# Performance work log

Measured on AMD Instinct MI355X. Metric: run time of the kernel, lower is better.

## Reference

```python
import jax, jax.numpy as jnp
import numpy as np
from jax import lax

W = 50      # window size
EPS = 1e-5  # BatchNorm eps (torch default)


def setup_inputs() -> dict:
    key = jax.random.key(0)
    ks = jax.random.split(key, 40)
    def n(i, shape, s=0.1):
        return (jax.random.normal(ks[i], shape, dtype=jnp.float32) * s).astype(jnp.float32)
    inp = {}
    inp['x'] = jax.random.normal(ks[0], (16, 1, 2048), dtype=jnp.float32)
    # conv stack (eval-mode BatchNorm: running mean/var are params)
    inp['conv1_w'] = n(1, (64, 1, 9));  inp['conv1_b'] = n(2, (64,))
    inp['bn1_g'] = 1.0 + n(3, (64,));   inp['bn1_b'] = n(4, (64,))
    inp['bn1_m'] = n(5, (64,));         inp['bn1_v'] = 0.5 + jax.random.uniform(ks[6], (64,), dtype=jnp.float32)
    inp['conv2_w'] = n(7, (32, 64, 7)); inp['conv2_b'] = n(8, (32,))
    inp['bn2_g'] = 1.0 + n(9, (32,));   inp['bn2_b'] = n(10, (32,))
    inp['bn2_m'] = n(11, (32,));        inp['bn2_v'] = 0.5 + jax.random.uniform(ks[12], (32,), dtype=jnp.float32)
    inp['conv3_w'] = n(13, (16, 32, 5)); inp['conv3_b'] = n(14, (16,))
    inp['bn3_g'] = 1.0 + n(15, (16,));   inp['bn3_b'] = n(16, (16,))
    inp['bn3_m'] = n(17, (16,));         inp['bn3_v'] = 0.5 + jax.random.uniform(ks[18], (16,), dtype=jnp.float32)
    # 2-layer LSTM, hidden 64, input 16 (torch gate order i,f,g,o)
    H = 64
    inp['wih0'] = n(19, (4 * H, 16)); inp['whh0'] = n(20, (4 * H, H))
    inp['bih0'] = n(21, (4 * H,));    inp['bhh0'] = n(22, (4 * H,))
    inp['wih1'] = n(23, (4 * H, H));  inp['whh1'] = n(24, (4 * H, H))
    inp['bih1'] = n(25, (4 * H,));    inp['bhh1'] = n(26, (4 * H,))
    # classifier 64 -> 32 -> 2
    inp['fc1_w'] = n(27, (32, H)); inp['fc1_b'] = n(28, (32,))
    inp['fc2_w'] = n(29, (2, 32)); inp['fc2_b'] = n(30, (2,))
    return inp


def _conv1d(x, w, b, pad):
    # x: [N, Cin, L], w: [Cout, Cin, K]
    y = lax.conv_general_dilated(x, w, (1,), [(pad, pad)],
                                 dimension_numbers=('NCH', 'OIH', 'NCH'))
    return y + b[:, None]


def _bn(x, g, b, m, v):
    # eval-mode BatchNorm1d over channel dim of [N, C, L]
    return (x - m[:, None]) * (g / jnp.sqrt(v + EPS))[:, None] + b[:, None]


def _lstm_layer(x, wih, whh, bih, bhh):
    # x: [B, T, D] -> [B, T, H]; torch gate order (i, f, g, o)
    B, T, D = x.shape
    H = whh.shape[1]
    xs = jnp.transpose(x, (1, 0, 2))                     # [T, B, D]
    pre = xs @ wih.T + (bih + bhh)                       # [T, B, 4H] input projection, hoisted
    def step(carry, p):
        h, c = carry
        g = p + h @ whh.T
        i, f, gg, o = jnp.split(g, 4, axis=-1)
        c = jax.nn.sigmoid(f) * c + jax.nn.sigmoid(i) * jnp.tanh(gg)
        h = jax.nn.sigmoid(o) * jnp.tanh(c)
        return (h, c), h
    h0 = jnp.zeros((B, H), x.dtype)
    _, hs = lax.scan(step, (h0, h0), pre)
    return jnp.transpose(hs, (1, 0, 2))


def reference(x, conv1_w, conv1_b, bn1_g, bn1_b, bn1_m, bn1_v,
              conv2_w, conv2_b, bn2_g, bn2_b, bn2_m, bn2_v,
              conv3_w, conv3_b, bn3_g, bn3_b, bn3_m, bn3_v,
              wih0, whh0, bih0, bhh0, wih1, whh1, bih1, bhh1,
              fc1_w, fc1_b, fc2_w, fc2_b):
    B, C, T = x.shape
    # sliding windows with left zero-pad of W-1 -> [B, T, C, W]
    xp = jnp.pad(x, ((0, 0), (0, 0), (W - 1, 0)))
    idx = jnp.arange(T)[:, None] + jnp.arange(W)[None, :]  # [T, W]
    win = xp[:, :, idx]                                    # [B, C, T, W]
    win = jnp.transpose(win, (0, 2, 1, 3)).reshape(B * T, C, W)
    # conv -> BN(eval) -> ReLU stack (dropout is identity in eval)
    h = jax.nn.relu(_bn(_conv1d(win, conv1_w, conv1_b, 4), bn1_g, bn1_b, bn1_m, bn1_v))
    h = jax.nn.relu(_bn(_conv1d(h, conv2_w, conv2_b, 3), bn2_g, bn2_b, bn2_m, bn2_v))
    h = jax.nn.relu(_bn(_conv1d(h, conv3_w, conv3_b, 2), bn3_g, bn3_b, bn3_m, bn3_v))
    feats = h.mean(axis=-1).reshape(B, T, -1)              # AdaptiveAvgPool1d(1) -> [B, T, 16]
    # 2-layer LSTM
    h1 = _lstm_layer(feats, wih0, whh0, bih0, bhh0)
    h2 = _lstm_layer(h1, wih1, whh1, bih1, bhh1)           # [B, T, 64]
    # classifier
    z = jax.nn.relu(h2 @ fc1_w.T + fc1_b)
    logits = z @ fc2_w.T + fc2_b                           # [B, T, 2]
    return logits
```

## Files before the change

### kernel.cpp

```cpp
#include <hip/hip_runtime.h>

#define EPSV 1e-5f
#define SCOPE_AGENT __HIP_MEMORY_SCOPE_AGENT

__device__ __forceinline__ float fast_rcp(float x) { return __builtin_amdgcn_rcpf(x); }
__device__ __forceinline__ float tanhfast(float x) {
    float e = __expf(2.0f * x);
    return 1.0f - 2.0f * fast_rcp(e + 1.0f);
}
__device__ __forceinline__ float dot4(const float4 w, const float4 v, float a) {
    a = fmaf(w.x, v.x, a);
    a = fmaf(w.y, v.y, a);
    a = fmaf(w.z, v.z, a);
    a = fmaf(w.w, v.w, a);
    return a;
}
#define DPPF(v, ctrl) __int_as_float(__builtin_amdgcn_mov_dpp(__float_as_int(v), (ctrl), 0xF, 0xF, false))

typedef unsigned long long ull;

struct Rec2S {
    float hbuf0[2][80];
    float hbuf1[2][80];
    float xst[16][80];
};
struct EdgeS {
    float A1[64 * 36];
    float A2[32 * 36];
    float xl[16], xr[16];
    float s1[64], t1[64], s2[32], t2[32], s3[16], t3[16];
    float psumE[288];
    float pi[512];
};

__global__ void pack_kernel(const float* __restrict__ w2, const float* __restrict__ w3,
                            float* __restrict__ w2t2, float4* __restrict__ w3p4,
                            float* __restrict__ w3p1, int* __restrict__ sync_ints) {
    int j = blockIdx.x * 256 + threadIdx.x;
    if (j < 16384) {
        int i = j >> 8;
        int o = (j >> 3) & 31;
        int k = j & 7;
        w2t2[j] = (k < 7) ? w2[o * 448 + i * 7 + k] : 0.0f;
    } else if (j < 16896) {
        int e = j - 16384;
        int i = e >> 4, o = e & 15;
        int base = o * 160 + i * 5;
        w3p4[e] = make_float4(w3[base], w3[base + 1], w3[base + 2], w3[base + 3]);
        w3p1[e] = w3[base + 4];
    } else if (j < 16896 + 4096) {
        sync_ints[j - 16896] = 0;
    }
}

__global__ __launch_bounds__(256) void conv1f_kernel(
    const float* __restrict__ x, const float* __restrict__ w1,
    const float* __restrict__ b1, const float* __restrict__ g1,
    const float* __restrict__ be1, const float* __restrict__ m1,
    const float* __restrict__ vv1, float* __restrict__ a1f)
{
    __shared__ float xs[72];
    const int tid = threadIdx.x;
    const int T = blockIdx.x * 64;
    const int b = blockIdx.y;
    if (tid < 72) {
        int gi = T - 49 + tid;
        xs[tid] = (gi >= 0 && gi < 2048) ? x[b * 2048 + gi] : 0.0f;
    }
    const int i = tid & 63, q = tid >> 6;
    float wv[9];
    #pragma unroll
    for (int k = 0; k < 9; ++k) wv[k] = w1[i * 9 + k];
    float sc = g1[i] * rsqrtf(vv1[i] + EPSV);
    float tc = (b1[i] - m1[i]) * sc + be1[i];
// ... 98 lines not shown
        float av[12] = {R0.x, R0.y, R0.z, R0.w, R1.x, R1.y, R1.z, R1.w,
                        R2.x, R2.y, R2.z, R2.w};
        float4 wa = w3p4[i * 16 + o];
        float w4 = w3p1[i * 16 + o];
        #pragma unroll
        for (int q = 0; q < 8; ++q) {
            acc[q] = fmaf(wa.x, av[q], acc[q]);
            acc[q] = fmaf(wa.y, av[q + 1], acc[q]);
            acc[q] = fmaf(wa.z, av[q + 2], acc[q]);
            acc[q] = fmaf(wa.w, av[q + 3], acc[q]);
            acc[q] = fmaf(w4,   av[q + 4], acc[q]);
        }
    }
    #pragma unroll
    for (int q = 0; q < 8; ++q) {
        int v3 = T + pg * 8 + q;
        if (v3 < 2079)
            a3f[((long)b * 2080 + v3) * 16 + o] = fmaxf(acc[q] * sc + tc, 0.0f);
        else if (v3 < 2080)
            a3f[((long)b * 2080 + v3) * 16 + o] = 0.0f;
    }
}

__device__ void rec_merged(char* smemraw, int b,
    const float* __restrict__ feats,
    const float* __restrict__ wih0, const float* __restrict__ whh0,
    const float* __restrict__ bih0, const float* __restrict__ bhh0,
    const float* __restrict__ wih1, const float* __restrict__ whh1,
    const float* __restrict__ bih1, const float* __restrict__ bhh1,
    float* __restrict__ h2o, int* __restrict__ cnt0)
{
    Rec2S* s = (Rec2S*)smemraw;
    const int tid = threadIdx.x;
    const int half = tid >> 8;
    const int lt = tid & 255;
    const int j = lt >> 2, kq = lt & 3;
    __builtin_amdgcn_s_setprio(1);

    const float* whh = half ? whh1 : whh0;
    const float* bih = half ? bih1 : bih0;
    const float* bhh = half ? bhh1 : bhh0;
    const float4* pa = (const float4*)(whh + (0 * 64 + j) * 64 + kq * 16);
    const float4* pb = (const float4*)(whh + (1 * 64 + j) * 64 + kq * 16);
    const float4* pc_ = (const float4*)(whh + (2 * 64 + j) * 64 + kq * 16);
    const float4* pd = (const float4*)(whh + (3 * 64 + j) * 64 + kq * 16);
    float4 A0 = pa[0], A1 = pa[1], A2 = pa[2], A3 = pa[3];
    float4 B0 = pb[0], B1 = pb[1], B2 = pb[2], B3 = pb[3];
    float4 C0 = pc_[0], C1 = pc_[1], C2 = pc_[2], C3 = pc_[3];
    float4 D0 = pd[0], D1 = pd[1], D2 = pd[2], D3 = pd[3];
    const float bb0 = bih[j] + bhh[j];
    const float bb1 = bih[64 + j] + bhh[64 + j];
    const float bb2 = bih[128 + j] + bhh[128 + j];
    const float bb3 = bih[192 + j] + bhh[192 + j];

    float4 z4 = make_float4(0.f, 0.f, 0.f, 0.f);
    float4 XA0 = z4, XA1 = z4, XA2 = z4, XA3 = z4;
    float4 XB0 = z4, XB1 = z4, XB2 = z4, XB3 = z4;
    float4 XC0 = z4, XC1 = z4, XC2 = z4, XC3 = z4;
    float4 XD0 = z4, XD1 = z4, XD2 = z4, XD3 = z4;
    float4 xw0 = z4, xw1 = z4, xw2 = z4, xw3 = z4;
// ... 21 lines not shown
    const float* fbase = feats + (long)b * 32768;
    __syncthreads();

#define LSTEP0(kk) \
    if (half == 0) { \
        const float4* hp_ = (const float4*)&s->hbuf0[((kk) + 1) & 1][kq * 20]; \
        float4 h0_ = hp_[0], h1_ = hp_[1], h2_ = hp_[2], h3_ = hp_[3]; \
        float4 xv_ = *(const float4*)&s->xst[(kk)][kq * 4]; \
        float p0 = dot4(A3, h3_, dot4(A2, h2_, dot4(A1, h1_, dot4(A0, h0_, dot4(xw0, xv_, 0.f))))); \
        float p1 = dot4(B3, h3_, dot4(B2, h2_, dot4(B1, h1_, dot4(B0, h0_, dot4(xw1, xv_, 0.f))))); \
        float p2 = dot4(C3, h3_, dot4(C2, h2_, dot4(C1, h1_, dot4(C0, h0_, dot4(xw2, xv_, 0.f))))); \
        float p3 = dot4(D3, h3_, dot4(D2, h2_, dot4(D1, h1_, dot4(D0, h0_, dot4(xw3, xv_, 0.f))))); \
        p0 += DPPF(p0, 0xB1); p1 += DPPF(p1, 0xB1); p2 += DPPF(p2, 0xB1); p3 += DPPF(p3, 0xB1); \
        p0 += DPPF(p0, 0x4E); p1 += DPPF(p1, 0x4E); p2 += DPPF(p2, 0x4E); p3 += DPPF(p3, 0x4E); \
        float gi = 1.0f - fast_rcp(__expf(p0 + bb0) + 1.0f); \
        float gf = 1.0f - fast_rcp(__expf(p1 + bb1) + 1.0f); \
        float gg = 1.0f - 2.0f * fast_rcp(__expf(2.0f * (p2 + bb2)) + 1.0f); \
        float go = 1.0f - fast_rcp(__expf(p3 + bb3) + 1.0f); \
        cst = fmaf(gf, cst, gi * gg); \
        float h_ = go * tanhfast(cst); \
        if (kq == 0) s->hbuf0[(kk) & 1][(j >> 4) * 20 + (j & 15)] = h_; \
    }

#define LSTEP1(mval, P) \
    if (half == 1 && (mval) >= 0) { \
        const float4* hp_ = (const float4*)&s->hbuf1[(P) ^ 1][kq * 20]; \
        float4 h0_ = hp_[0], h1_ = hp_[1], h2_ = hp_[2], h3_ = hp_[3]; \
        const float4* xp_ = (const float4*)&s->hbuf0[(P)][kq * 20]; \
        float4 x0_ = xp_[0], x1_ = xp_[1], x2_ = xp_[2], x3_ = xp_[3]; \
        float p0 = dot4(A3, h3_, dot4(A2, h2_, dot4(A1, h1_, dot4(A0, h0_, \
                   dot4(XA3, x3_, dot4(XA2, x2_, dot4(XA1, x1_, dot4(XA0, x0_, 0.f)))))))); \
        float p1 = dot4(B3, h3_, dot4(B2, h2_, dot4(B1, h1_, dot4(B0, h0_, \
                   dot4(XB3, x3_, dot4(XB2, x2_, dot4(XB1, x1_, dot4(XB0, x0_, 0.f)))))))); \
        float p2 = dot4(C3, h3_, dot4(C2, h2_, dot4(C1, h1_, dot4(C0, h0_, \
                   dot4(XC3, x3_, dot4(XC2, x2_, dot4(XC1, x1_, dot4(XC0, x0_, 0.f)))))))); \
        float p3 = dot4(D3, h3_, dot4(D2, h2_, dot4(D1, h1_, dot4(D0, h0_, \
                   dot4(XD3, x3_, dot4(XD2, x2_, dot4(XD1, x1_, dot4(XD0, x0_, 0.f)))))))); \
        p0 += DPPF(p0, 0xB1); p1 += DPPF(p1, 0xB1); p2 += DPPF(p2, 0xB1); p3 += DPPF(p3, 0xB1); \
        p0 += DPPF(p0, 0x4E); p1 += DPPF(p1, 0x4E); p2 += DPPF(p2, 0x4E); p3 += DPPF(p3, 0x4E); \
        float gi = 1.0f - fast_rcp(__expf(p0 + bb0) + 1.0f); \
        float gf = 1.0f - fast_rcp(__expf(p1 + bb1) + 1.0f); \
        float gg = 1.0f - 2.0f * fast_rcp(__expf(2.0f * (p2 + bb2)) + 1.0f); \
        float go = 1.0f - fast_rcp(__expf(p3 + bb3) + 1.0f); \
        cst = fmaf(gf, cst, gi * gg); \
        float h_ = go * tanhfast(cst); \
        if (kq == 0) { \
            s->hbuf1[(P)][(j >> 4) * 20 + (j & 15)] = h_; \
            h2o[((long)b * 2048 + (mval)) * 64 + j] = h_; \
        } \
    }

    for (int c = 0; c < 128; ++c) {
        const int gb = c * 16;
        if (tid == 0) {
            while (__hip_atomic_load(&cnt0[b * 128 + c], __ATOMIC_RELAXED, SCOPE_AGENT) < 16)
                __builtin_amdgcn_s_sleep(2);
        }
        __syncthreads();
        if (half == 0)
            s->xst[lt >> 4][lt & 15] =
                __hip_atomic_load(fbase + c * 256 + lt, __ATOMIC_RELAXED, SCOPE_AGENT);
        LSTEP1(gb - 1, 1)
        __syncthreads();
        LSTEP0(0)                       __syncthreads();
        LSTEP0(1)   LSTEP1(gb + 0, 0)  __syncthreads();
        LSTEP0(2)   LSTEP1(gb + 1, 1)  __syncthreads();
        LSTEP0(3)   LSTEP1(gb + 2, 0)  __syncthreads();
        LSTEP0(4)   LSTEP1(gb + 3, 1)  __syncthreads();
        LSTEP0(5)   LSTEP1(gb + 4, 0)  __syncthreads();
        LSTEP0(6)   LSTEP1(gb + 5, 1)  __syncthreads();
        LSTEP0(7)   LSTEP1(gb + 6, 0)  __syncthreads();
        LSTEP0(8)   LSTEP1(gb + 7, 1)  __syncthreads();
        LSTEP0(9)   LSTEP1(gb + 8, 0)  __syncthreads();
        LSTEP0(10)  LSTEP1(gb + 9, 1)  __syncthreads();
        LSTEP0(11)  LSTEP1(gb + 10, 0) __syncthreads();
        LSTEP0(12)  LSTEP1(gb + 11, 1) __syncthreads();
        LSTEP0(13)  LSTEP1(gb + 12, 0) __syncthreads();
        LSTEP0(14)  LSTEP1(gb + 13, 1) __syncthreads();
        LSTEP0(15)  LSTEP1(gb + 14, 0) __syncthreads();
    }
    LSTEP1(2047, 1)
#undef LSTEP0
#undef LSTEP1
}

__device__ void edge_worker2(char* smemraw, int w,
    const float* __restrict__ x,
    const float* __restrict__ w1,
    const float* __restrict__ b1, const float* __restrict__ g1,
    const float* __restrict__ be1, const float* __restrict__ m1, const float* __restrict__ vv1,
    const float* __restrict__ b2, const float* __restrict__ g2,
    const float* __restrict__ be2, const float* __restrict__ m2, const float* __restrict__ vv2,
    const float* __restrict__ b3, const float* __restrict__ g3,
    const float* __restrict__ be3, const float* __restrict__ m3, const float* __restrict__ vv3,
    const float* __restrict__ w2t2,
    const float4* __restrict__ w3p4, const float* __restrict__ w3p1,
    const float* __restrict__ a1f, const float* __restrict__ a2f,
    const float* __restrict__ a3f,
    float* __restrict__ feats, int* __restrict__ cnt0)
{
    const int half = threadIdx.x >> 8;
    EdgeS* s = ((EdgeS*)smemraw) + half;
    const int tid = threadIdx.x & 255;

    for (int idx = tid; idx < 1088; idx += 256) {
        if (idx < 768) {
            int row = idx / 12, z = idx - row * 12;
            int slot = (z < 3) ? z : (z < 6 ? 10 + z : 20 + z);
            s->A1[row * 36 + slot] = 0.0f;
        } else {
            int e = idx - 768;
            int row = e / 10, z = e - row * 10;
            int slot = (z < 2) ? z : (z < 5 ? 11 + z : 22 + z);
            s->A2[row * 36 + slot] = 0.0f;
        }
    }
    if (tid < 64) {
        float sc = g1[tid] * rsqrtf(vv1[tid] + EPSV);
        s->s1[tid] = sc;
        s->t1[tid] = (b1[tid] - m1[tid]) * sc + be1[tid];
    } else if (tid < 96) {
        int o = tid - 64;
        float sc = g2[o] * rsqrtf(vv2[o] + EPSV);
        s->s2[o] = sc;
        s->t2[o] = (b2[o] - m2[o]) * sc + be2[o];
    } else if (tid < 112) {
        int o = tid - 96;
        float sc = g3[o] * rsqrtf(vv3[o] + EPSV);
        s->s3[o] = sc;
        s->t3[o] = (b3[o] - m3[o]) * sc + be3[o];
    }
    const int o1 = tid >> 2, g1q = tid & 3;
    float wv[9];
    #pragma unroll
    for (int k = 0; k < 9; ++k) wv[k] = w1[o1 * 9 + k];
    __syncthreads();
    const float sc1 = s->s1[o1], tc1 = s->t1[o1];

    for (int it = 0; it < 69; ++it) {
        int tile = it * 480 + 2 * w + half;
        bool active = tile < 32768;
        int tt = active ? tile : 32767;
        const int b = tt & 15, t = tt >> 4;

        if (tid < 128) {
            int dv = tid >> 2, o4 = (tid & 3) * 4;
            *(float4*)&s->pi[dv * 16 + o4] =
                *(const float4*)&a3f[((long)b * 2080 + t + dv) * 16 + o4];
        }
        if (tid >= 112 && tid < 128) {
            int m = tid - 112;
            float v = 0.0f;
            if (m >= 4) { int gi = t - 53 + m; if (gi >= 0) v = x[b * 2048 + gi]; }
            s->xl[m] = v;
        } else if (tid >= 128 && tid < 144) {
            int m = tid - 128;
            float v = 0.0f;
            if (m <= 7) { int gi = t - 7 + m; if (gi >= 0) v = x[b * 2048 + gi]; }
            s->xr[m] = v;
        }
        {
            if (tid < 96) {
                int d = tid >> 4, i4 = (tid & 15) * 4;
                float4 f = *(const float4*)&a1f[((long)b * 2089 + t + d) * 64 + i4];
                int slot = 7 + d;
                s->A1[(i4 + 0) * 36 + slot] = f.x;
                s->A1[(i4 + 1) * 36 + slot] = f.y;
                s->A1[(i4 + 2) * 36 + slot] = f.z;
                s->A1[(i4 + 3) * 36 + slot] = f.w;
            } else if (tid < 192) {
                int e = tid - 96;
                int d = e >> 4, i4 = (e & 15) * 4;
                float4 f = *(const float4*)&a1f[((long)b * 2089 + t + 36 + d) * 64 + i4];
                int slot = 16 + d;
                s->A1[(i4 + 0) * 36 + slot] = f.x;
                s->A1[(i4 + 1) * 36 + slot] = f.y;
                s->A1[(i4 + 2) * 36 + slot] = f.z;
                s->A1[(i4 + 3) * 36 + slot] = f.w;
            } else if (tid < 224) {
                int e = tid - 192;
                int d = e >> 3, i4 = (e & 7) * 4;
                float4 f = *(const float4*)&a2f[((long)b * 2083 + t + d) * 32 + i4];
                int slot = 9 + d;
                s->A2[(i4 + 0) * 36 + slot] = f.x;
                s->A2[(i4 + 1) * 36 + slot] = f.y;
                s->A2[(i4 + 2) * 36 + slot] = f.z;
                s->A2[(i4 + 3) * 36 + slot] = f.w;
            } else {
                int e = tid - 224;
                int d = e >> 3, i4 = (e & 7) * 4;
                float4 f = *(const float4*)&a2f[((long)b * 2083 + t + 32 + d) * 32 + i4];
                int slot = 16 + d;
                s->A2[(i4 + 0) * 36 + slot] = f.x;
                s->A2[(i4 + 1) * 36 + slot] = f.y;
                s->A2[(i4 + 2) * 36 + slot] = f.z;
                s->A2[(i4 + 3) * 36 + slot] = f.w;
            }
        }
        __syncthreads();

        {
            float accL = 0.0f, accR = 0.0f;
            #pragma unroll
            for (int k = 0; k < 9; ++k) {
                accL = fmaf(wv[k], s->xl[g1q + k], accL);
                accR = fmaf(wv[k], s->xr[g1q + k], accR);
            }
            s->A1[o1 * 36 + 3 + g1q]  = fmaxf(accL * sc1 + tc1, 0.0f);
            s->A1[o1 * 36 + 22 + g1q] = fmaxf(accR * sc1 + tc1, 0.0f);
        }
        __syncthreads();

        {
            const int o = tid >> 3, side = (tid >> 2) & 1, isub = tid & 3;
            const int sbase = side * 16;
            float acc[7];
            #pragma unroll
            for (int q = 0; q < 7; ++q) acc[q] = 0.0f;
            #pragma unroll 2
            for (int ii = 0; ii < 16; ++ii) {
                int i = 4 * ii + isub;
                const float* rp = &s->A1[i * 36 + sbase];
                float4 R0 = *(const float4*)&rp[0];
                float4 R1 = *(const float4*)&rp[4];
                float4 R2 = *(const float4*)&rp[8];
                float r12 = rp[12];
                float av[13] = {R0.x, R0.y, R0.z, R0.w, R1.x, R1.y, R1.z, R1.w,
                                R2.x, R2.y, R2.z, R2.w, r12};
                const float4* wp = (const float4*)&w2t2[(i * 32 + o) * 8];
                float4 Wa = wp[0], Wb = wp[1];
                float wk[7] = {Wa.x, Wa.y, Wa.z, Wa.w, Wb.x, Wb.y, Wb.z};
                #pragma unroll
                for (int k = 0; k < 7; ++k) {
                    #pragma unroll
                    for (int q = 0; q < 7; ++q) acc[q] = fmaf(wk[k], av[q + k], acc[q]);
                }
            }
            #pragma unroll
            for (int q = 0; q < 7; ++q) {
                acc[q] += DPPF(acc[q], 0xB1);
                acc[q] += DPPF(acc[q], 0x4E);
            }
            if (isub == 0) {
                float sc = s->s2[o], tc = s->t2[o];
                #pragma unroll
                for (int q = 0; q < 7; ++q) {
                    float r = fmaxf(acc[q] * sc + tc, 0.0f);
                    s->A2[o * 36 + (side ? 20 + q : 2 + q)] = r;
                }
            }
        }
        __syncthreads();

        {
            const int o = (tid >> 2) & 15, isub = tid & 3;
            const int side = (tid >> 6) & 1, pg = tid >> 7;
            float acc[5];
            #pragma unroll
            for (int n = 0; n < 5; ++n) acc[n] = 0.0f;
            if (pg == 0) {
                #pragma unroll 2
                for (int ii = 0; ii < 8; ++ii) {
                    int i = 4 * ii + isub;
                    const float* rp = &s->A2[i * 36 + side * 16];
                    float4 R0 = *(const float4*)&rp[0];
                    float4 R1 = *(const float4*)&rp[4];
                    float t8 = rp[8];
                    float av[9] = {R0.x, R0.y, R0.z, R0.w, R1.x, R1.y, R1.z, R1.w, t8};
                    float4 wa = w3p4[i * 16 + o];
                    float w4 = w3p1[i * 16 + o];
                    #pragma unroll
                    for (int n = 0; n < 5; ++n) {
                        acc[n] = fmaf(wa.x, av[n], acc[n]);
                        acc[n] = fmaf(wa.y, av[n + 1], acc[n]);
                        acc[n] = fmaf(wa.z, av[n + 2], acc[n]);
                        acc[n] = fmaf(wa.w, av[n + 3], acc[n]);
                        acc[n] = fmaf(w4,   av[n + 4], acc[n]);
                    }
                }
            } else {
                #pragma unroll 2
                for (int ii = 0; ii < 8; ++ii) {
                    int i = 4 * ii + isub;
                    const float* rp = &s->A2[i * 36 + side * 16];
                    float4 R1 = *(const float4*)&rp[4];
                    float4 R2 = *(const float4*)&rp[8];
                    float t12 = rp[12];
                    float av[8] = {R1.y, R1.z, R1.w, R2.x, R2.y, R2.z, R2.w, t12};
                    float4 wa = w3p4[i * 16 + o];
                    float w4 = w3p1[i * 16 + o];
                    #pragma unroll
                    for (int n = 0; n < 4; ++n) {
                        acc[n] = fmaf(wa.x, av[n], acc[n]);
                        acc[n] = fmaf(wa.y, av[n + 1], acc[n]);
                        acc[n] = fmaf(wa.z, av[n + 2], acc[n]);
                        acc[n] = fmaf(wa.w, av[n + 3], acc[n]);
                        acc[n] = fmaf(w4,   av[n + 4], acc[n]);
                    }
                }
            }
            #pragma unroll
            for (int n = 0; n < 5; ++n) {
                acc[n] += DPPF(acc[n], 0xB1);
                acc[n] += DPPF(acc[n], 0x4E);
            }
            if (isub == 0) {
                float sc = s->s3[o], tc = s->t3[o];
                if (pg == 0) {
                    #pragma unroll
                    for (int n = 0; n < 5; ++n)
                        s->psumE[(side * 9 + n) * 16 + o] = fmaxf(acc[n] * sc + tc, 0.0f);
                } else {
                    #pragma unroll
                    for (int n = 0; n < 4; ++n)
                        s->psumE[(side * 9 + 5 + n) * 16 + o] = fmaxf(acc[n] * sc + tc, 0.0f);
                }
            }
        }
        __syncthreads();

        if (tid < 16 && active) {
            float e = 0.0f;
            #pragma unroll
            for (int P3 = 0; P3 < 18; ++P3) e += s->psumE[P3 * 16 + tid];
            float ii = 0.0f;
            #pragma unroll
            for (int dv = 0; dv < 32; ++dv) ii += s->pi[dv * 16 + tid];
            __hip_atomic_store(&feats[((long)b * 2048 + t) * 16 + tid], (e + ii) * (1.0f / 50.0f),
                               __ATOMIC_RELAXED, SCOPE_AGENT);
        }
        __syncthreads();
        if (tid == 0 && active)
            __hip_atomic_fetch_add(&cnt0[b * 128 + (t >> 4)], 1, __ATOMIC_RELAXED, SCOPE_AGENT);
    }
}

__global__ __launch_bounds__(512, 2) void fused_kernel(
    const float* __restrict__ x,
    const float* __restrict__ w1, const float* __restrict__ b1,
    const float* __restrict__ g1, const float* __restrict__ be1,
    const float* __restrict__ m1, const float* __restrict__ vv1,
    const float* __restrict__ b2,
    const float* __restrict__ g2, const float* __restrict__ be2,
    const float* __restrict__ m2, const float* __restrict__ vv2,
    const float* __restrict__ b3,
    const float* __restrict__ g3, const float* __restrict__ be3,
    const float* __restrict__ m3, const float* __restrict__ vv3,
    const float* __restrict__ w2t2,
    const float4* __restrict__ w3p4, const float* __restrict__ w3p1,
    const float* __restrict__ a1f, const float* __restrict__ a2f,
    const float* __restrict__ a3f,
    const float* __restrict__ wih0, const float* __restrict__ whh0,
    const float* __restrict__ bih0, const float* __restrict__ bhh0,
    const float* __restrict__ wih1, const float* __restrict__ whh1,
    const float* __restrict__ bih1, const float* __restrict__ bhh1,
    float* __restrict__ feats, float* __restrict__ h2o,
    int* __restrict__ cnt0)
{
    __shared__ __align__(16) char smem[sizeof(EdgeS) * 2 > sizeof(Rec2S) ? sizeof(EdgeS) * 2 : sizeof(Rec2S)];

    const int bid = blockIdx.x;
    if (bid < 16) {
        rec_merged(smem, bid, feats, wih0, whh0, bih0, bhh0,
                   wih1, whh1, bih1, bhh1, h2o, cnt0);
        return;
    }
    edge_worker2(smem, bid - 16, x, w1, b1, g1, be1, m1, vv1, b2, g2, be2, m2, vv2,
                 b3, g3, be3, m3, vv3, w2t2, w3p4, w3p1, a1f, a2f, a3f, feats, cnt0);
}

__global__ __launch_bounds__(256) void fc_kernel(
    const float* __restrict__ h2o,
    const float* __restrict__ fc1w, const float* __restrict__ fc1b,
    const float* __restrict__ fc2w, const float* __restrict__ fc2b,
    float* __restrict__ out)
{
    int r = blockIdx.x * 256 + threadIdx.x;
    float h[64];
    const float4* hp = (const float4*)(h2o + (long)r * 64);
    #pragma unroll
    for (int i = 0; i < 16; ++i) {
        float4 v = hp[i];
        h[4 * i] = v.x; h[4 * i + 1] = v.y; h[4 * i + 2] = v.z; h[4 * i + 3] = v.w;
    }
    float l0 = fc2b[0], l1 = fc2b[1];
    #pragma unroll 4
    for (int j = 0; j < 32; ++j) {
        float z = fc1b[j];
        #pragma unroll
        for (int k = 0; k < 64; ++k) z = fmaf(h[k], fc1w[j * 64 + k], z);
        z = fmaxf(z, 0.0f);
// ... 26 lines not shown
    const float* be3  = (const float*)d_in[16];
    const float* m3   = (const float*)d_in[17];
    const float* v3   = (const float*)d_in[18];
    const float* wih0 = (const float*)d_in[19];
    const float* whh0 = (const float*)d_in[20];
    const float* bih0 = (const float*)d_in[21];
    const float* bhh0 = (const float*)d_in[22];
    const float* wih1 = (const float*)d_in[23];
    const float* whh1 = (const float*)d_in[24];
    const float* bih1 = (const float*)d_in[25];
    const float* bhh1 = (const float*)d_in[26];
    const float* fc1w = (const float*)d_in[27];
    const float* fc1b = (const float*)d_in[28];
    const float* fc2w = (const float*)d_in[29];
    const float* fc2b = (const float*)d_in[30];
    float* out = (float*)d_out;

    float* ws    = (float*)d_ws;
    float* feats = ws;
    float* h2o   = feats + 32768 * 16;
    float* w2t2  = h2o + 32768 * 64;
    float* w3p4f = w2t2 + 16384;
    float* w3p1  = w3p4f + 2048;
    float* h1o   = w3p1 + 512;
    float* a1f   = h1o + 32768 * 64;
    float* a2f   = a1f + 16 * 2089 * 64;
    float* a3f   = a2f + 16 * 2083 * 32;
    int*   cnt0  = (int*)(a3f + 16 * 2080 * 16);
    (void)in_sizes; (void)n_in; (void)out_size; (void)ws_size;

    hipLaunchKernelGGL(pack_kernel, dim3(82), dim3(256), 0, stream,
                       w2, w3, w2t2, (float4*)w3p4f, w3p1, cnt0);
    hipLaunchKernelGGL(conv1f_kernel, dim3(33, 16), dim3(256), 0, stream,
                       x, w1, b1, g1, be1, m1, v1, a1f);
    hipLaunchKernelGGL(conv2f_kernel, dim3(33, 16), dim3(256), 0, stream,
                       a1f, w2t2, b2, g2, be2, m2, v2, a2f);
    hipLaunchKernelGGL(conv3f_kernel, dim3(17, 16), dim3(256), 0, stream,
                       a2f, (const float4*)w3p4f, w3p1, b3, g3, be3, m3, v3, a3f);
    hipLaunchKernelGGL(fused_kernel, dim3(256), dim3(512), 0, stream,
                       x, w1, b1, g1, be1, m1, v1, b2, g2, be2, m2, v2,
                       b3, g3, be3, m3, v3, w2t2, (const float4*)w3p4f, w3p1,
                       a1f, a2f, a3f,
                       wih0, whh0, bih0, bhh0, wih1, whh1, bih1, bhh1,
                       feats, h2o, cnt0);
    hipLaunchKernelGGL(fc_kernel, dim3(128), dim3(256), 0, stream,
                       h2o, fc1w, fc1b, fc2w, fc2b, out);
}
```

Before: 1.312 ms.

## Split fused producer/consumer kernel into separate edge and recurrence kernels

Result: slower. 1.907 ms (+45.3%).

```diff
diff --git a/kernel.cpp b/kernel.cpp
--- a/kernel.cpp
+++ b/kernel.cpp
@@ -1,7 +1,6 @@
 #include <hip/hip_runtime.h>
 
 #define EPSV 1e-5f
-#define SCOPE_AGENT __HIP_MEMORY_SCOPE_AGENT
 
 __device__ __forceinline__ float fast_rcp(float x) { return __builtin_amdgcn_rcpf(x); }
 __device__ __forceinline__ float tanhfast(float x) {
@@ -22,6 +21,7 @@
 struct Rec2S {
     float hbuf0[2][80];
     float hbuf1[2][80];
+    float ring[16][64];
     float xst[16][80];
 };
 struct EdgeS {
@@ -35,7 +35,7 @@
 
 __global__ void pack_kernel(const float* __restrict__ w2, const float* __restrict__ w3,
                             float* __restrict__ w2t2, float4* __restrict__ w3p4,
-                            float* __restrict__ w3p1, int* __restrict__ sync_ints) {
+                            float* __restrict__ w3p1) {
     int j = blockIdx.x * 256 + threadIdx.x;
     if (j < 16384) {
         int i = j >> 8;
@@ -48,8 +48,6 @@
         int base = o * 160 + i * 5;
         w3p4[e] = make_float4(w3[base], w3[base + 1], w3[base + 2], w3[base + 3]);
         w3p1[e] = w3[base + 4];
-    } else if (j < 16896 + 4096) {
-        sync_ints[j - 16896] = 0;
     }
 }
 
@@ -194,20 +192,260 @@
     }
 }
 
-__device__ void rec_merged(char* smemraw, int b,
+__global__ __launch_bounds__(256, 4) void edges_kernel(
+    const float* __restrict__ x,
+    const float* __restrict__ w1,
+    const float* __restrict__ b1, const float* __restrict__ g1,
+    const float* __restrict__ be1, const float* __restrict__ m1, const float* __restrict__ vv1,
+    const float* __restrict__ b2, const float* __restrict__ g2,
+    const float* __restrict__ be2, const float* __restrict__ m2, const float* __restrict__ vv2,
+    const float* __restrict__ b3, const float* __restrict__ g3,
+    const float* __restrict__ be3, const float* __restrict__ m3, const float* __restrict__ vv3,
+    const float* __restrict__ w2t2,
+    const float4* __restrict__ w3p4, const float* __restrict__ w3p1,
+    const float* __restrict__ a1f, const float* __restrict__ a2f,
+    const float* __restrict__ a3f,
+    float* __restrict__ feats)
+{
+    __shared__ __align__(16) char smemraw[sizeof(EdgeS)];
+    EdgeS* s = (EdgeS*)smemraw;
+    const int tid = threadIdx.x;
+    const int b = blockIdx.x >> 11;
+    const int t = blockIdx.x & 2047;
+
+    for (int idx = tid; idx < 1088; idx += 256) {
+        if (idx < 768) {
+            int row = idx / 12, z = idx - row * 12;
+            int slot = (z < 3) ? z : (z < 6 ? 10 + z : 20 + z);
+            s->A1[row * 36 + slot] = 0.0f;
+        } else {
+            int e = idx - 768;
+            int row = e / 10, z = e - row * 10;
+            int slot = (z < 2) ? z : (z < 5 ? 11 + z : 22 + z);
+            s->A2[row * 36 + slot] = 0.0f;
+        }
+    }
+    if (tid < 128) {
+        int dv = tid >> 2, o4 = (tid & 3) * 4;
+        *(float4*)&s->pi[dv * 16 + o4] =
+            *(const float4*)&a3f[((long)b * 2080 + t + dv) * 16 + o4];
+    }
+    if (tid < 64) {
+        float sc = g1[tid] * rsqrtf(vv1[tid] + EPSV);
+        s->s1[tid] = sc;
+        s->t1[tid] = (b1[tid] - m1[tid]) * sc + be1[tid];
+    } else if (tid < 96) {
+        int o = tid - 64;
+        float sc = g2[o] * rsqrtf(vv2[o] + EPSV);
+        s->s2[o] = sc;
+        s->t2[o] = (b2[o] - m2[o]) * sc + be2[o];
+    } else if (tid < 112) {
+        int o = tid - 96;
+        float sc = g3[o] * rsqrtf(vv3[o] + EPSV);
+        s->s3[o] = sc;
+        s->t3[o] = (b3[o] - m3[o]) * sc + be3[o];
+    } else if (tid < 128) {
+        int m = tid - 112;
+        float v = 0.0f;
+        if (m >= 4) { int gi = t - 53 + m; if (gi >= 0) v = x[b * 2048 + gi]; }
+        s->xl[m] = v;
+    } else if (tid < 144) {
+        int m = tid - 128;
+        float v = 0.0f;
+        if (m <= 7) { int gi = t - 7 + m; if (gi >= 0) v = x[b * 2048 + gi]; }
+        s->xr[m] = v;
+    }
+    {
+        if (tid < 96) {
+            int d = tid >> 4, i4 = (tid & 15) * 4;
+            float4 f = *(const float4*)&a1f[((long)b * 2089 + t + d) * 64 + i4];
+            int slot = 7 + d;
+            s->A1[(i4 + 0) * 36 + slot] = f.x;
+            s->A1[(i4 + 1) * 36 + slot] = f.y;
+            s->A1[(i4 + 2) * 36 + slot] = f.z;
+            s->A1[(i4 + 3) * 36 + slot] = f.w;
+        } else if (tid < 192) {
+            int e = tid - 96;
+            int d = e >> 4, i4 = (e & 15) * 4;
+            float4 f = *(const float4*)&a1f[((long)b * 2089 + t + 36 + d) * 64 + i4];
+            int slot = 16 + d;
+            s->A1[(i4 + 0) * 36 + slot] = f.x;
+            s->A1[(i4 + 1) * 36 + slot] = f.y;
+            s->A1[(i4 + 2) * 36 + slot] = f.z;
+            s->A1[(i4 + 3) * 36 + slot] = f.w;
+        } else if (tid < 224) {
+            int e = tid - 192;
+            int d = e >> 3, i4 = (e & 7) * 4;
+            float4 f = *(const float4*)&a2f[((long)b * 2083 + t + d) * 32 + i4];
+            int slot = 9 + d;
+            s->A2[(i4 + 0) * 36 + slot] = f.x;
+            s->A2[(i4 + 1) * 36 + slot] = f.y;
+            s->A2[(i4 + 2) * 36 + slot] = f.z;
+            s->A2[(i4 + 3) * 36 + slot] = f.w;
+        } else {
+            int e = tid - 224;
+            int d = e >> 3, i4 = (e & 7) * 4;
+            float4 f = *(const float4*)&a2f[((long)b * 2083 + t + 32 + d) * 32 + i4];
+            int slot = 16 + d;
+            s->A2[(i4 + 0) * 36 + slot] = f.x;
+            s->A2[(i4 + 1) * 36 + slot] = f.y;
+            s->A2[(i4 + 2) * 36 + slot] = f.z;
+            s->A2[(i4 + 3) * 36 + slot] = f.w;
+        }
+    }
+    __syncthreads();
+
+    {
+        const int o = tid >> 2, g = tid & 3;
+        float wv[9];
+        #pragma unroll
+        for (int k = 0; k < 9; ++k) wv[k] = w1[o * 9 + k];
+        float accL = 0.0f, accR = 0.0f;
+        #pragma unroll
+        for (int k = 0; k < 9; ++k) {
+            accL = fmaf(wv[k], s->xl[g + k], accL);
+            accR = fmaf(wv[k], s->xr[g + k], accR);
+        }
+        float sc = s->s1[o], tc = s->t1[o];
+        s->A1[o * 36 + 3 + g]  = fmaxf(accL * sc + tc, 0.0f);
+        s->A1[o * 36 + 22 + g] = fmaxf(accR * sc + tc, 0.0f);
+    }
+    __syncthreads();
+
+    {
+        const int o = tid >> 3, side = (tid >> 2) & 1, isub = tid & 3;
+        const int sbase = side * 16;
+        float acc[7];
+        #pragma unroll
+        for (int q = 0; q < 7; ++q) acc[q] = 0.0f;
+        #pragma unroll 2
+        for (int ii = 0; ii < 16; ++ii) {
+            int i = 4 * ii + isub;
+            const float* rp = &s->A1[i * 36 + sbase];
+            float4 R0 = *(const float4*)&rp[0];
+            float4 R1 = *(const float4*)&rp[4];
+            float4 R2 = *(const float4*)&rp[8];
+            float r12 = rp[12];
+            float av[13] = {R0.x, R0.y, R0.z, R0.w, R1.x, R1.y, R1.z, R1.w,
+                            R2.x, R2.y, R2.z, R2.w, r12};
+            const float4* wp = (const float4*)&w2t2[(i * 32 + o) * 8];
+            float4 Wa = wp[0], Wb = wp[1];
+            float wk[7] = {Wa.x, Wa.y, Wa.z, Wa.w, Wb.x, Wb.y, Wb.z};
+            #pragma unroll
+            for (int k = 0; k < 7; ++k) {
+                #pragma unroll
+                for (int q = 0; q < 7; ++q) acc[q] = fmaf(wk[k], av[q + k], acc[q]);
+            }
+        }
+        #pragma unroll
+        for (int q = 0; q < 7; ++q) {
+            acc[q] += DPPF(acc[q], 0xB1);
+            acc[q] += DPPF(acc[q], 0x4E);
+        }
+        if (isub == 0) {
+            float sc = s->s2[o], tc = s->t2[o];
+            #pragma unroll
+            for (int q = 0; q < 7; ++q) {
+                float r = fmaxf(acc[q] * sc + tc, 0.0f);
+                s->A2[o * 36 + (side ? 20 + q : 2 + q)] = r;
+            }
+        }
+    }
+    __syncthreads();
+
+    {
+        const int o = (tid >> 2) & 15, isub = tid & 3;
+        const int side = (tid >> 6) & 1, pg = tid >> 7;
+        float acc[5];
+        #pragma unroll
+        for (int n = 0; n < 5; ++n) acc[n] = 0.0f;
+        if (pg == 0) {
+            #pragma unroll 2
+            for (int ii = 0; ii < 8; ++ii) {
+                int i = 4 * ii + isub;
+                const float* rp = &s->A2[i * 36 + side * 16];
+                float4 R0 = *(const float4*)&rp[0];
+                float4 R1 = *(const float4*)&rp[4];
+                float t8 = rp[8];
+                float av[9] = {R0.x, R0.y, R0.z, R0.w, R1.x, R1.y, R1.z, R1.w, t8};
+                float4 wa = w3p4[i * 16 + o];
+                float w4 = w3p1[i * 16 + o];
+                #pragma unroll
+                for (int n = 0; n < 5; ++n) {
+                    acc[n] = fmaf(wa.x, av[n], acc[n]);
+                    acc[n] = fmaf(wa.y, av[n + 1], acc[n]);
+                    acc[n] = fmaf(wa.z, av[n + 2], acc[n]);
+                    acc[n] = fmaf(wa.w, av[n + 3], acc[n]);
+                    acc[n] = fmaf(w4,   av[n + 4], acc[n]);
+                }
+            }
+        } else {
+            #pragma unroll 2
+            for (int ii = 0; ii < 8; ++ii) {
+                int i = 4 * ii + isub;
+                const float* rp = &s->A2[i * 36 + side * 16];
+                float4 R1 = *(const float4*)&rp[4];
+                float4 R2 = *(const float4*)&rp[8];
+                float t12 = rp[12];
+                float av[8] = {R1.y, R1.z, R1.w, R2.x, R2.y, R2.z, R2.w, t12};
+                float4 wa = w3p4[i * 16 + o];
+                float w4 = w3p1[i * 16 + o];
+                #pragma unroll
+                for (int n = 0; n < 4; ++n) {
+                    acc[n] = fmaf(wa.x, av[n], acc[n]);
+                    acc[n] = fmaf(wa.y, av[n + 1], acc[n]);
+                    acc[n] = fmaf(wa.z, av[n + 2], acc[n]);
+                    acc[n] = fmaf(wa.w, av[n + 3], acc[n]);
+                    acc[n] = fmaf(w4,   av[n + 4], acc[n]);
+                }
+            }
+        }
+        #pragma unroll
+        for (int n = 0; n < 5; ++n) {
+            acc[n] += DPPF(acc[n], 0xB1);
+            acc[n] += DPPF(acc[n], 0x4E);
+        }
+        if (isub == 0) {
+            float sc = s->s3[o], tc = s->t3[o];
+            if (pg == 0) {
+                #pragma unroll
+                for (int n = 0; n < 5; ++n)
+                    s->psumE[(side * 9 + n) * 16 + o] = fmaxf(acc[n] * sc + tc, 0.0f);
+            } else {
+                #pragma unroll
+                for (int n = 0; n < 4; ++n)
+                    s->psumE[(side * 9 + 5 + n) * 16 + o] = fmaxf(acc[n] * sc + tc, 0.0f);
+            }
+        }
+    }
+    __syncthreads();
+
+    if (tid < 16) {
+        float e = 0.0f;
+        #pragma unroll
+        for (int P3 = 0; P3 < 18; ++P3) e += s->psumE[P3 * 16 + tid];
+        float ii = 0.0f;
+        #pragma unroll
+        for (int dv = 0; dv < 32; ++dv) ii += s->pi[dv * 16 + tid];
+        feats[((long)b * 2048 + t) * 16 + tid] = (e + ii) * (1.0f / 50.0f);
+    }
+}
+
+__global__ __launch_bounds__(512, 2) void rec_kernel(
     const float* __restrict__ feats,
     const float* __restrict__ wih0, const float* __restrict__ whh0,
     const float* __restrict__ bih0, const float* __restrict__ bhh0,
     const float* __restrict__ wih1, const float* __restrict__ whh1,
     const float* __restrict__ bih1, const float* __restrict__ bhh1,
-    float* __restrict__ h2o, int* __restrict__ cnt0)
+    float* __restrict__ h2o)
 {
+    __shared__ __align__(16) char smemraw[sizeof(Rec2S)];
     Rec2S* s = (Rec2S*)smemraw;
+    const int b = blockIdx.x;
     const int tid = threadIdx.x;
     const int half = tid >> 8;
     const int lt = tid & 255;
     const int j = lt >> 2, kq = lt & 3;
-    __builtin_amdgcn_s_setprio(1);
 
     const float* whh = half ? whh1 : whh0;
     const float* bih = half ? bih1 : bih0;
@@ -275,7 +513,7 @@
         if (kq == 0) s->hbuf0[(kk) & 1][(j >> 4) * 20 + (j & 15)] = h_; \
     }
 
-#define LSTEP1(mval, P) \
+#define LSTEP1(mval, P, S) \
     if (half == 1 && (mval) >= 0) { \
         const float4* hp_ = (const float4*)&s->hbuf1[(P) ^ 1][kq * 20]; \
         float4 h0_ = hp_[0], h1_ = hp_[1], h2_ = hp_[2], h3_ = hp_[3]; \
@@ -299,327 +537,47 @@
         float h_ = go * tanhfast(cst); \
         if (kq == 0) { \
             s->hbuf1[(P)][(j >> 4) * 20 + (j & 15)] = h_; \
-            h2o[((long)b * 2048 + (mval)) * 64 + j] = h_; \
+            s->ring[(S)][j] = h_; \
         } \
     }
 
     for (int c = 0; c < 128; ++c) {
         const int gb = c * 16;
-        if (tid == 0) {
-            while (__hip_atomic_load(&cnt0[b * 128 + c], __ATOMIC_RELAXED, SCOPE_AGENT) < 16)
-                __builtin_amdgcn_s_sleep(2);
-        }
+        if (half == 0)
+            s->xst[lt >> 4][lt & 15] = fbase[c * 256 + lt];
+        LSTEP1(gb - 1, 1, 0)
         __syncthreads();
-        if (half == 0)
-            s->xst[lt >> 4][lt & 15] =
-                __hip_atomic_load(fbase + c * 256 + lt, __ATOMIC_RELAXED, SCOPE_AGENT);
-        LSTEP1(gb - 1, 1)
+        LSTEP0(0)                           __syncthreads();
+        LSTEP0(1)   LSTEP1(gb + 0, 0, 1)   __syncthreads();
+        LSTEP0(2)   LSTEP1(gb + 1, 1, 2)   __syncthreads();
+        LSTEP0(3)   LSTEP1(gb + 2, 0, 3)   __syncthreads();
+        LSTEP0(4)   LSTEP1(gb + 3, 1, 4)   __syncthreads();
+        LSTEP0(5)   LSTEP1(gb + 4, 0, 5)   __syncthreads();
+        LSTEP0(6)   LSTEP1(gb + 5, 1, 6)   __syncthreads();
+        LSTEP0(7)   LSTEP1(gb + 6, 0, 7)   __syncthreads();
+        LSTEP0(8)   LSTEP1(gb + 7, 1, 8)   __syncthreads();
+        LSTEP0(9)   LSTEP1(gb + 8, 0, 9)   __syncthreads();
+        LSTEP0(10)  LSTEP1(gb + 9, 1, 10)  __syncthreads();
+        LSTEP0(11)  LSTEP1(gb + 10, 0, 11) __syncthreads();
+        LSTEP0(12)  LSTEP1(gb + 11, 1, 12) __syncthreads();
+        LSTEP0(13)  LSTEP1(gb + 12, 0, 13) __syncthreads();
+        LSTEP0(14)  LSTEP1(gb + 13, 1, 14) __syncthreads();
+        LSTEP0(15)  LSTEP1(gb + 14, 0, 15) __syncthreads();
+        {
+            int e0 = tid, e1 = tid + 512;
+            int r0 = e0 >> 6, i0 = e0 & 63;
+            int r1 = e1 >> 6, i1 = e1 & 63;
+            int m0 = gb - 1 + r0, m1 = gb - 1 + r1;
+            if (m0 >= 0) h2o[((long)b * 2048 + m0) * 64 + i0] = s->ring[r0][i0];
+            h2o[((long)b * 2048 + m1) * 64 + i1] = s->ring[r1][i1];
+        }
         __syncthreads();
-        LSTEP0(0)                       __syncthreads();
-        LSTEP0(1)   LSTEP1(gb + 0, 0)  __syncthreads();
-        LSTEP0(2)   LSTEP1(gb + 1, 1)  __syncthreads();
-        LSTEP0(3)   LSTEP1(gb + 2, 0)  __syncthreads();
-        LSTEP0(4)   LSTEP1(gb + 3, 1)  __syncthreads();
-        LSTEP0(5)   LSTEP1(gb + 4, 0)  __syncthreads();
-        LSTEP0(6)   LSTEP1(gb + 5, 1)  __syncthreads();
-        LSTEP0(7)   LSTEP1(gb + 6, 0)  __syncthreads();
-        LSTEP0(8)   LSTEP1(gb + 7, 1)  __syncthreads();
-        LSTEP0(9)   LSTEP1(gb + 8, 0)  __syncthreads();
-        LSTEP0(10)  LSTEP1(gb + 9, 1)  __syncthreads();
-        LSTEP0(11)  LSTEP1(gb + 10, 0) __syncthreads();
-        LSTEP0(12)  LSTEP1(gb + 11, 1) __syncthreads();
-        LSTEP0(13)  LSTEP1(gb + 12, 0) __syncthreads();
-        LSTEP0(14)  LSTEP1(gb + 13, 1) __syncthreads();
-        LSTEP0(15)  LSTEP1(gb + 14, 0) __syncthreads();
-    }
-    LSTEP1(2047, 1)
+    }
+    LSTEP1(2047, 1, 0)
+    __syncthreads();
+    if (tid < 64) h2o[((long)b * 2048 + 2047) * 64 + tid] = s->ring[0][tid];
 #undef LSTEP0
 #undef LSTEP1
-}
-
-__device__ void edge_worker2(char* smemraw, int w,
-    const float* __restrict__ x,
-    const float* __restrict__ w1,
-    const float* __restrict__ b1, const float* __restrict__ g1,
-    const float* __restrict__ be1, const float* __restrict__ m1, const float* __restrict__ vv1,
-    const float* __restrict__ b2, const float* __restrict__ g2,
-    const float* __restrict__ be2, const float* __restrict__ m2, const float* __restrict__ vv2,
-    const float* __restrict__ b3, const float* __restrict__ g3,
-    const float* __restrict__ be3, const float* __restrict__ m3, const float* __restrict__ vv3,
-    const float* __restrict__ w2t2,
-    const float4* __restrict__ w3p4, const float* __restrict__ w3p1,
-    const float* __restrict__ a1f, const float* __restrict__ a2f,
-    const float* __restrict__ a3f,
-    float* __restrict__ feats, int* __restrict__ cnt0)
-{
-    const int half = threadIdx.x >> 8;
-    EdgeS* s = ((EdgeS*)smemraw) + half;
-    const int tid = threadIdx.x & 255;
-
-    for (int idx = tid; idx < 1088; idx += 256) {
-        if (idx < 768) {
-            int row = idx / 12, z = idx - row * 12;
-            int slot = (z < 3) ? z : (z < 6 ? 10 + z : 20 + z);
-            s->A1[row * 36 + slot] = 0.0f;
-        } else {
-            int e = idx - 768;
-            int row = e / 10, z = e - row * 10;
-            int slot = (z < 2) ? z : (z < 5 ? 11 + z : 22 + z);
-            s->A2[row * 36 + slot] = 0.0f;
-        }
-    }
-    if (tid < 64) {
-        float sc = g1[tid] * rsqrtf(vv1[tid] + EPSV);
-        s->s1[tid] = sc;
-        s->t1[tid] = (b1[tid] - m1[tid]) * sc + be1[tid];
-    } else if (tid < 96) {
-        int o = tid - 64;
-        float sc = g2[o] * rsqrtf(vv2[o] + EPSV);
-        s->s2[o] = sc;
-        s->t2[o] = (b2[o] - m2[o]) * sc + be2[o];
-    } else if (tid < 112) {
-        int o = tid - 96;
-        float sc = g3[o] * rsqrtf(vv3[o] + EPSV);
-        s->s3[o] = sc;
-        s->t3[o] = (b3[o] - m3[o]) * sc + be3[o];
-    }
-    const int o1 = tid >> 2, g1q = tid & 3;
-    float wv[9];
-    #pragma unroll
-    for (int k = 0; k < 9; ++k) wv[k] = w1[o1 * 9 + k];
-    __syncthreads();
-    const float sc1 = s->s1[o1], tc1 = s->t1[o1];
-
-    for (int it = 0; it < 69; ++it) {
-        int tile = it * 480 + 2 * w + half;
-        bool active = tile < 32768;
-        int tt = active ? tile : 32767;
-        const int b = tt & 15, t = tt >> 4;
-
-        if (tid < 128) {
-            int dv = tid >> 2, o4 = (tid & 3) * 4;
-            *(float4*)&s->pi[dv * 16 + o4] =
-                *(const float4*)&a3f[((long)b * 2080 + t + dv) * 16 + o4];
-        }
-        if (tid >= 112 && tid < 128) {
-            int m = tid - 112;
-            float v = 0.0f;
-            if (m >= 4) { int gi = t - 53 + m; if (gi >= 0) v = x[b * 2048 + gi]; }
-            s->xl[m] = v;
-        } else if (tid >= 128 && tid < 144) {
-            int m = tid - 128;
-            float v = 0.0f;
-            if (m <= 7) { int gi = t - 7 + m; if (gi >= 0) v = x[b * 2048 + gi]; }
-            s->xr[m] = v;
-        }
-        {
-            if (tid < 96) {
-                int d = tid >> 4, i4 = (tid & 15) * 4;
-                float4 f = *(const float4*)&a1f[((long)b * 2089 + t + d) * 64 + i4];
-                int slot = 7 + d;
-                s->A1[(i4 + 0) * 36 + slot] = f.x;
-                s->A1[(i4 + 1) * 36 + slot] = f.y;
-                s->A1[(i4 + 2) * 36 + slot] = f.z;
-                s->A1[(i4 + 3) * 36 + slot] = f.w;
-            } else if (tid < 192) {
-                int e = tid - 96;
-                int d = e >> 4, i4 = (e & 15) * 4;
-                float4 f = *(const float4*)&a1f[((long)b * 2089 + t + 36 + d) * 64 + i4];
-                int slot = 16 + d;
-                s->A1[(i4 + 0) * 36 + slot] = f.x;
-                s->A1[(i4 + 1) * 36 + slot] = f.y;
-                s->A1[(i4 + 2) * 36 + slot] = f.z;
-                s->A1[(i4 + 3) * 36 + slot] = f.w;
-            } else if (tid < 224) {
-                int e = tid - 192;
-                int d = e >> 3, i4 = (e & 7) * 4;
-                float4 f = *(const float4*)&a2f[((long)b * 2083 + t + d) * 32 + i4];
-                int slot = 9 + d;
-                s->A2[(i4 + 0) * 36 + slot] = f.x;
-                s->A2[(i4 + 1) * 36 + slot] = f.y;
-                s->A2[(i4 + 2) * 36 + slot] = f.z;
-                s->A2[(i4 + 3) * 36 + slot] = f.w;
-            } else {
-                int e = tid - 224;
-                int d = e >> 3, i4 = (e & 7) * 4;
-                float4 f = *(const float4*)&a2f[((long)b * 2083 + t + 32 + d) * 32 + i4];
-                int slot = 16 + d;
-                s->A2[(i4 + 0) * 36 + slot] = f.x;
-                s->A2[(i4 + 1) * 36 + slot] = f.y;
-                s->A2[(i4 + 2) * 36 + slot] = f.z;
-                s->A2[(i4 + 3) * 36 + slot] = f.w;
-            }
-        }
-        __syncthreads();
-
-        {
-            float accL = 0.0f, accR = 0.0f;
-            #pragma unroll
-            for (int k = 0; k < 9; ++k) {
-                accL = fmaf(wv[k], s->xl[g1q + k], accL);
-                accR = fmaf(wv[k], s->xr[g1q + k], accR);
-            }
-            s->A1[o1 * 36 + 3 + g1q]  = fmaxf(accL * sc1 + tc1, 0.0f);
-            s->A1[o1 * 36 + 22 + g1q] = fmaxf(accR * sc1 + tc1, 0.0f);
-        }
-        __syncthreads();
-
-        {
-            const int o = tid >> 3, side = (tid >> 2) & 1, isub = tid & 3;
-            const int sbase = side * 16;
-            float acc[7];
-            #pragma unroll
-            for (int q = 0; q < 7; ++q) acc[q] = 0.0f;
-            #pragma unroll 2
-            for (int ii = 0; ii < 16; ++ii) {
-                int i = 4 * ii + isub;
-                const float* rp = &s->A1[i * 36 + sbase];
-                float4 R0 = *(const float4*)&rp[0];
-                float4 R1 = *(const float4*)&rp[4];
-                float4 R2 = *(const float4*)&rp[8];
-                float r12 = rp[12];
-                float av[13] = {R0.x, R0.y, R0.z, R0.w, R1.x, R1.y, R1.z, R1.w,
-                                R2.x, R2.y, R2.z, R2.w, r12};
-                const float4* wp = (const float4*)&w2t2[(i * 32 + o) * 8];
-                float4 Wa = wp[0], Wb = wp[1];
-                float wk[7] = {Wa.x, Wa.y, Wa.z, Wa.w, Wb.x, Wb.y, Wb.z};
-                #pragma unroll
-                for (int k = 0; k < 7; ++k) {
-                    #pragma unroll
-                    for (int q = 0; q < 7; ++q) acc[q] = fmaf(wk[k], av[q + k], acc[q]);
-                }
-            }
-            #pragma unroll
-            for (int q = 0; q < 7; ++q) {
-                acc[q] += DPPF(acc[q], 0xB1);
-                acc[q] += DPPF(acc[q], 0x4E);
-            }
-            if (isub == 0) {
-                float sc = s->s2[o], tc = s->t2[o];
-                #pragma unroll
-                for (int q = 0; q < 7; ++q) {
-                    float r = fmaxf(acc[q] * sc + tc, 0.0f);
-                    s->A2[o * 36 + (side ? 20 + q : 2 + q)] = r;
-                }
-            }
-        }
-        __syncthreads();
-
-        {
-            const int o = (tid >> 2) & 15, isub = tid & 3;
-            const int side = (tid >> 6) & 1, pg = tid >> 7;
-            float acc[5];
-            #pragma unroll
-            for (int n = 0; n < 5; ++n) acc[n] = 0.0f;
-            if (pg == 0) {
-                #pragma unroll 2
-                for (int ii = 0; ii < 8; ++ii) {
-                    int i = 4 * ii + isub;
-                    const float* rp = &s->A2[i * 36 + side * 16];
-                    float4 R0 = *(const float4*)&rp[0];
-                    float4 R1 = *(const float4*)&rp[4];
-                    float t8 = rp[8];
-                    float av[9] = {R0.x, R0.y, R0.z, R0.w, R1.x, R1.y, R1.z, R1.w, t8};
-                    float4 wa = w3p4[i * 16 + o];
-                    float w4 = w3p1[i * 16 + o];
-                    #pragma unroll
-                    for (int n = 0; n < 5; ++n) {
-                        acc[n] = fmaf(wa.x, av[n], acc[n]);
-                        acc[n] = fmaf(wa.y, av[n + 1], acc[n]);
-                        acc[n] = fmaf(wa.z, av[n + 2], acc[n]);
-                        acc[n] = fmaf(wa.w, av[n + 3], acc[n]);
-                        acc[n] = fmaf(w4,   av[n + 4], acc[n]);
-                    }
-                }
-            } else {
-                #pragma unroll 2
-                for (int ii = 0; ii < 8; ++ii) {
-                    int i = 4 * ii + isub;
-                    const float* rp = &s->A2[i * 36 + side * 16];
-                    float4 R1 = *(const float4*)&rp[4];
-                    float4 R2 = *(const float4*)&rp[8];
-                    float t12 = rp[12];
-                    float av[8] = {R1.y, R1.z, R1.w, R2.x, R2.y, R2.z, R2.w, t12};
-                    float4 wa = w3p4[i * 16 + o];
-                    float w4 = w3p1[i * 16 + o];
-                    #pragma unroll
-                    for (int n = 0; n < 4; ++n) {
-                        acc[n] = fmaf(wa.x, av[n], acc[n]);
-                        acc[n] = fmaf(wa.y, av[n + 1], acc[n]);
-                        acc[n] = fmaf(wa.z, av[n + 2], acc[n]);
-                        acc[n] = fmaf(wa.w, av[n + 3], acc[n]);
-                        acc[n] = fmaf(w4,   av[n + 4], acc[n]);
-                    }
-                }
-            }
-            #pragma unroll
-            for (int n = 0; n < 5; ++n) {
-                acc[n] += DPPF(acc[n], 0xB1);
-                acc[n] += DPPF(acc[n], 0x4E);
-            }
-            if (isub == 0) {
-                float sc = s->s3[o], tc = s->t3[o];
-                if (pg == 0) {
-                    #pragma unroll
-                    for (int n = 0; n < 5; ++n)
-                        s->psumE[(side * 9 + n) * 16 + o] = fmaxf(acc[n] * sc + tc, 0.0f);
-                } else {
-                    #pragma unroll
-                    for (int n = 0; n < 4; ++n)
-                        s->psumE[(side * 9 + 5 + n) * 16 + o] = fmaxf(acc[n] * sc + tc, 0.0f);
-                }
-            }
-        }
-        __syncthreads();
-
-        if (tid < 16 && active) {
-            float e = 0.0f;
-            #pragma unroll
-            for (int P3 = 0; P3 < 18; ++P3) e += s->psumE[P3 * 16 + tid];
-            float ii = 0.0f;
-            #pragma unroll
-            for (int dv = 0; dv < 32; ++dv) ii += s->pi[dv * 16 + tid];
-            __hip_atomic_store(&feats[((long)b * 2048 + t) * 16 + tid], (e + ii) * (1.0f / 50.0f),
-                               __ATOMIC_RELAXED, SCOPE_AGENT);
-        }
-        __syncthreads();
-        if (tid == 0 && active)
-            __hip_atomic_fetch_add(&cnt0[b * 128 + (t >> 4)], 1, __ATOMIC_RELAXED, SCOPE_AGENT);
-    }
-}
-
-__global__ __launch_bounds__(512, 2) void fused_kernel(
-    const float* __restrict__ x,
-    const float* __restrict__ w1, const float* __restrict__ b1,
-    const float* __restrict__ g1, const float* __restrict__ be1,
-    const float* __restrict__ m1, const float* __restrict__ vv1,
-    const float* __restrict__ b2,
-    const float* __restrict__ g2, const float* __restrict__ be2,
-    const float* __restrict__ m2, const float* __restrict__ vv2,
-    const float* __restrict__ b3,
-    const float* __restrict__ g3, const float* __restrict__ be3,
-    const float* __restrict__ m3, const float* __restrict__ vv3,
-    const float* __restrict__ w2t2,
-    const float4* __restrict__ w3p4, const float* __restrict__ w3p1,
-    const float* __restrict__ a1f, const float* __restrict__ a2f,
-    const float* __restrict__ a3f,
-    const float* __restrict__ wih0, const float* __restrict__ whh0,
-    const float* __restrict__ bih0, const float* __restrict__ bhh0,
-    const float* __restrict__ wih1, const float* __restrict__ whh1,
-    const float* __restrict__ bih1, const float* __restrict__ bhh1,
-    float* __restrict__ feats, float* __restrict__ h2o,
-    int* __restrict__ cnt0)
-{
-    __shared__ __align__(16) char smem[sizeof(EdgeS) * 2 > sizeof(Rec2S) ? sizeof(EdgeS) * 2 : sizeof(Rec2S)];
-
-    const int bid = blockIdx.x;
-    if (bid < 16) {
-        rec_merged(smem, bid, feats, wih0, whh0, bih0, bhh0,
-                   wih1, whh1, bih1, bhh1, h2o, cnt0);
-        return;
-    }
-    edge_worker2(smem, bid - 16, x, w1, b1, g1, be1, m1, vv1, b2, g2, be2, m2, vv2,
-                 b3, g3, be3, m3, vv3, w2t2, w3p4, w3p1, a1f, a2f, a3f, feats, cnt0);
 }
 
 __global__ __launch_bounds__(256) void fc_kernel(
@@ -692,27 +650,25 @@
     float* w2t2  = h2o + 32768 * 64;
     float* w3p4f = w2t2 + 16384;
     float* w3p1  = w3p4f + 2048;
-    float* h1o   = w3p1 + 512;
-    float* a1f   = h1o + 32768 * 64;
+    float* a1f   = w3p1 + 512;
     float* a2f   = a1f + 16 * 2089 * 64;
     float* a3f   = a2f + 16 * 2083 * 32;
-    int*   cnt0  = (int*)(a3f + 16 * 2080 * 16);
     (void)in_sizes; (void)n_in; (void)out_size; (void)ws_size;
 
-    hipLaunchKernelGGL(pack_kernel, dim3(82), dim3(256), 0, stream,
-                       w2, w3, w2t2, (float4*)w3p4f, w3p1, cnt0);
+    hipLaunchKernelGGL(pack_kernel, dim3(66), dim3(256), 0, stream,
+                       w2, w3, w2t2, (float4*)w3p4f, w3p1);
     hipLaunchKernelGGL(conv1f_kernel, dim3(33, 16), dim3(256), 0, stream,
                        x, w1, b1, g1, be1, m1, v1, a1f);
     hipLaunchKernelGGL(conv2f_kernel, dim3(33, 16), dim3(256), 0, stream,
                        a1f, w2t2, b2, g2, be2, m2, v2, a2f);
     hipLaunchKernelGGL(conv3f_kernel, dim3(17, 16), dim3(256), 0, stream,
                        a2f, (const float4*)w3p4f, w3p1, b3, g3, be3, m3, v3, a3f);
-    hipLaunchKernelGGL(fused_kernel, dim3(256), dim3(512), 0, stream,
+    hipLaunchKernelGGL(edges_kernel, dim3(32768), dim3(256), 0, stream,
                        x, w1, b1, g1, be1, m1, v1, b2, g2, be2, m2, v2,
                        b3, g3, be3, m3, v3, w2t2, (const float4*)w3p4f, w3p1,
-                       a1f, a2f, a3f,
-                       wih0, whh0, bih0, bhh0, wih1, whh1, bih1, bhh1,
-                       feats, h2o, cnt0);
+                       a1f, a2f, a3f, feats);
+    hipLaunchKernelGGL(rec_kernel, dim3(16), dim3(512), 0, stream,
+                       feats, wih0, whh0, bih0, bhh0, wih1, whh1, bih1, bhh1, h2o);
     hipLaunchKernelGGL(fc_kernel, dim3(128), dim3(256), 0, stream,
                        h2o, fc1w, fc1b, fc2w, fc2b, out);
 }
```
